# Optimization experiments

Measured on AMD Instinct MI355X. Metric: run time of the kernel, lower is better.

Reference implementation:

```python
import jax, jax.numpy as jnp
import numpy as np

# ---- static config (mirrors init_kwargs) ----
H, N, HKV = 32, 64, 8
HN = H * N            # model dim 2048
KV_DIM = HKV * N      # 512
B, T = 2, 1024
EPS = 1e-6
ROPE_THETA = 1.0e6
SPLITS_WAVGK = (96, 96, 64, 256, 64)   # xw, xa, xv, xg, xk lora ranks
SPLITS_RKV = (HN, KV_DIM, KV_DIM)


def rms_norm(x, w, eps=EPS):
    xf = x.astype(jnp.float32)
    var = jnp.mean(xf * xf, axis=-1, keepdims=True)
    return (w * (xf * jax.lax.rsqrt(var + eps))).astype(x.dtype)


def rotate_half(x):
    x1, x2 = jnp.split(x, 2, axis=-1)
    return jnp.concatenate((-x2, x1), axis=-1)


def apply_rope(q, k, cos, sin):
    # q:[B,T,H,N], k:[B,T,HKV,N], cos/sin:[B,T,N] -> unsqueeze head dim (unsqueeze_dim=2)
    cos = cos[:, :, None, :]
    sin = sin[:, :, None, :]
    return q * cos + rotate_half(q) * sin, k * cos + rotate_half(k) * sin


def rwkv7_recurrence(r, gk, k, v, a, b, S0):
    # fused_recurrent_rwkv7 (head_first=False). All inputs [B,T,H,N] fp32, S0 [B,H,N_key,N_val].
    # S_t = diag(exp(gk_t)) S_{t-1} + b_t (a_t^T S_{t-1}) + k_t v_t^T ;  o_t = r_t^T S_t
    def step(S, inp):
        r_t, w_t, k_t, v_t, a_t, b_t = inp
        sa = jnp.einsum('bhk,bhkv->bhv', a_t, S)
        S = (jnp.exp(w_t)[..., None] * S
             + k_t[..., None] * v_t[..., None, :]
             + b_t[..., None] * sa[..., None, :])
        o = jnp.einsum('bhk,bhkv->bhv', r_t, S)
        return S, o
    xs = tuple(jnp.swapaxes(t, 0, 1) for t in (r, gk, k, v, a, b))  # [T,B,H,N]
    S, o = jax.lax.scan(step, S0, xs)
    return jnp.swapaxes(o, 0, 1), S


def setup_inputs() -> dict:
    key = jax.random.key(0)
    ks = jax.random.split(key, 24)
    f32 = jnp.float32
    rn = lambda k, shape, s=1.0: jax.random.normal(k, shape, dtype=f32) * s

    x_in = rn(ks[0], (B, T, HN))
    v_first = rn(ks[1], (B, T, HKV, N))
    k_first = rn(ks[2], (B, T, HKV, N))
    state = jnp.zeros((B, H, N, N), f32)

    # real rope cache (faithful to get_batch_rope_cache output) at positions 0..T-1
    inv_freq = 1.0 / (ROPE_THETA ** (np.arange(0, N, 2, dtype=np.float32) / N))
    freqs = np.outer(np.arange(T, dtype=np.float32), inv_freq)  # [T, N/2]
    emb = np.concatenate([freqs, freqs], axis=-1)               # [T, N]
    calc_cos = jnp.broadcast_to(jnp.asarray(np.cos(emb), dtype=np.float32), (B, T, N))
    calc_sin = jnp.broadcast_to(jnp.asarray(np.sin(emb), dtype=np.float32), (B, T, N))

    wavgk1 = rn(ks[3], (HN, sum(SPLITS_WAVGK)), 0.02)
    w0 = rn(ks[4], (HN,), 0.5)
    w2 = rn(ks[5], (SPLITS_WAVGK[0], HN), 0.02)
    a0 = rn(ks[6], (HN,), 0.1)
    a2 = rn(ks[7], (SPLITS_WAVGK[1], HN), 0.02)
    v0 = rn(ks[8], (KV_DIM,), 0.1)
    v2 = rn(ks[9], (SPLITS_WAVGK[2], KV_DIM), 0.02)
    g2 = rn(ks[10], (SPLITS_WAVGK[3], HN), 0.02)
    k0 = rn(ks[11], (KV_DIM,), 0.1)
    k2 = rn(ks[12], (SPLITS_WAVGK[4], KV_DIM), 0.02)
    r_k = rn(ks[13], (H, N), 0.1)
    RKV = rn(ks[14], (HN, HN + 2 * KV_DIM), 0.02)   # fpx weight, dequantized form
    O = rn(ks[15], (HN, HN), 0.02)
    R_bias = rn(ks[16], (HN,), 0.02)
    K_bias = rn(ks[17], (KV_DIM,), 0.02)
    V_bias = rn(ks[18], (KV_DIM,), 0.02)
    ln_r = jnp.ones((N,), f32)
    ln_k = jnp.ones((N,), f32)
    ln1 = jnp.ones((HN,), f32)
    ln2 = jnp.ones((HN,), f32)

    return dict(x_in=x_in, v_first=v_first, k_first=k_first, state=state,
                calc_cos=calc_cos, calc_sin=calc_sin, wavgk1=wavgk1,
                w0=w0, w2=w2, a0=a0, a2=a2, v0=v0, v2=v2, g2=g2, k0=k0, k2=k2,
                r_k=r_k, RKV=RKV, O=O, R_bias=R_bias, K_bias=K_bias, V_bias=V_bias,
                ln_r=ln_r, ln_k=ln_k, ln1=ln1, ln2=ln2)


def reference(x_in, v_first, k_first, state, calc_cos, calc_sin, wavgk1,
              w0, w2, a0, a2, v0, v2, g2, k0, k2, r_k, RKV, O,
              R_bias, K_bias, V_bias, ln_r, ln_k, ln1, ln2):
    Bx, Tx, C = x_in.shape
    kv_repeat = HN // KV_DIM  # GQA repeat factor (4)

    x = rms_norm(x_in, ln1)
    xw, xa, xv, xg, xk = jnp.split(x @ wavgk1, np.cumsum(SPLITS_WAVGK)[:-1].tolist(), axis=-1)

    rkv = x @ RKV  # fpx_matmul -> dense matmul on dequantized weight
    r, k, v = jnp.split(rkv, np.cumsum(SPLITS_RKV)[:-1].tolist(), axis=-1)
    r = (r + R_bias).reshape(Bx, Tx, H, N)
    k = (k + K_bias).reshape(Bx, Tx, HKV, N)
    v = (v + V_bias).reshape(Bx, Tx, HKV, N)

    r = rms_norm(r, ln_r)
    k = rms_norm(k, ln_k)
    r, k = apply_rope(r, k, calc_cos, calc_sin)

    # layer_id = 1 (> 0): mix with first-layer value/key
    v = v + (v_first - v) * jax.nn.sigmoid(xv @ v2 + v0).reshape(Bx, Tx, HKV, N)
    k = k + (k_first - k) * jax.nn.sigmoid(xk @ k2 + k0).reshape(Bx, Tx, HKV, N)

    # repeat_kv: [B,T,HKV,N] -> [B,T,H,N] -> [B,T,HN]
    k = jnp.repeat(k, kv_repeat, axis=2).reshape(Bx, Tx, HN)
    v = jnp.repeat(v, kv_repeat, axis=2).reshape(Bx, Tx, HN)

    a = jax.nn.sigmoid(xa @ a2 + a0)  # in-context learning rate gate [B,T,HN]
    k4 = k.reshape(Bx, Tx, H, N)
    kk = (k4 / jnp.maximum(jnp.linalg.norm(k4, axis=-1, keepdims=True), 1e-12)).reshape(Bx, Tx, HN)

    w_log = -jax.nn.softplus(-(jnp.tanh(xw) @ w2 + w0)) - 0.5  # log-decay, <= -0.5
    k = k * (1.0 - w_log + a)
    aa = -kk
    bb = kk * a
    gk = -jnp.exp(w_log.astype(jnp.float32))  # passed to fused_recurrent_rwkv7 as log decay

    shp = (Bx, Tx, H, N)
    o, state_out = rwkv7_recurrence(
        r.reshape(shp).astype(jnp.float32), gk.reshape(shp),
        k.reshape(shp).astype(jnp.float32), v.reshape(shp).astype(jnp.float32),
        aa.reshape(shp).astype(jnp.float32), bb.reshape(shp).astype(jnp.float32),
        state.astype(jnp.float32))

    xx = o.reshape(Bx, Tx, HN) * (float(N) ** -0.5)
    bonus = ((r * k.reshape(shp) * r_k).sum(axis=-1, keepdims=True) * v.reshape(shp)).reshape(Bx, Tx, HN)
    xx = xx.astype(x_in.dtype) + bonus

    out = (xx * (jax.nn.sigmoid(xg) @ g2)) @ O  # fpx output projection
    x_new = x_in + out
    return rms_norm(x_new, ln2)
```

## Files before the change

kernel.cpp:

```cpp
#include <hip/hip_runtime.h>

typedef unsigned short u16;
typedef unsigned int u32;

using f32x4 = __attribute__((ext_vector_type(4))) float;
using bf16x8 = __attribute__((ext_vector_type(8))) __bf16;

#define HN 2048
#define KVD 512
#define TOKENS 2048
#define N1 3712
#define K2W 576
#define N2 7168

#define OFF_Y1   0ull
#define OFF_OO   0ull
#define OFF_XG   16777216ull
#define OFF_Y2   30408704ull
#define OFF_OUTR 30408704ull
#define OFF_BT1  89128960ull
#define OFF_XB   104333312ull
#define OFF_W2T  89128960ull
#define OFF_X2   97386496ull
#define OFF_OT   89128960ull
#define OFF_RR   112721920ull
#define OFF_DEC  129499136ull
#define OFF_KR   146276352ull
#define OFF_VV   163053568ull
#define OFF_AA   179830784ull
#define OFF_BB   196608000ull
#define OFF_PAB  213385216ull
#define OFF_PKR  230162432ull
#define WS_NEED  246939648ull

__device__ __forceinline__ u16 f2bf(float f) {
    u32 u = __float_as_uint(f);
    u32 r = u + 0x7fffu + ((u >> 16) & 1u);
    return (u16)(r >> 16);
}
__device__ __forceinline__ float sigm(float x) { return 1.f / (1.f + expf(-x)); }
__device__ __forceinline__ float wsum(float v) {
#pragma unroll
    for (int m = 32; m > 0; m >>= 1) v += __shfl_xor(v, m, 64);
    return v;
}
__device__ __forceinline__ float rowsum16(float v) {
    float t;
    t = __uint_as_float(__builtin_amdgcn_update_dpp(0, __float_as_uint(v), 0x121, 0xf, 0xf, true));
    v += t;
    t = __uint_as_float(__builtin_amdgcn_update_dpp(0, __float_as_uint(v), 0x122, 0xf, 0xf, true));
    v += t;
    t = __uint_as_float(__builtin_amdgcn_update_dpp(0, __float_as_uint(v), 0x124, 0xf, 0xf, true));
    v += t;
    t = __uint_as_float(__builtin_amdgcn_update_dpp(0, __float_as_uint(v), 0x128, 0xf, 0xf, true));
    v += t;
    return v;
}

typedef __attribute__((address_space(1))) const void glob_t;
typedef __attribute__((address_space(3))) void lds_t;
__device__ __forceinline__ void gload_lds16(const void* g, void* l) {
    __builtin_amdgcn_global_load_lds((glob_t*)g, (lds_t*)l, 16, 0, 0);
}

template<int OFF>
__device__ __forceinline__ float4 ds_read128(u32 a) {
    float4 r;
    asm volatile("ds_read_b128 %0, %1 offset:%2" : "=v"(r) : "v"(a), "i"(OFF));
    return r;
}
template<int OFF>
__device__ __forceinline__ uint4 ds_read128u(u32 a) {
    uint4 r;
    asm volatile("ds_read_b128 %0, %1 offset:%2" : "=v"(r) : "v"(a), "i"(OFF));
    return r;
}
template<int OFF>
__device__ __forceinline__ float ds_read32(u32 a) {
    float r;
    asm volatile("ds_read_b32 %0, %1 offset:%2" : "=v"(r) : "v"(a), "i"(OFF));
    return r;
}

__global__ __launch_bounds__(256) void k_prep_bt1(const float* __restrict__ wavgk1,
                                                  const float* __restrict__ RKV,
                                                  u16* __restrict__ BT1) {
    __shared__ float tile[64][65];
    const int bn = blockIdx.x >> 5;
    const int bk = blockIdx.x & 31;
    const int n0 = bn << 6, k0 = bk << 6;
    const int c = threadIdx.x & 63, q = threadIdx.x >> 6;
#pragma unroll
    for (int i = 0; i < 16; ++i) {
        const int r = (q << 4) + i;
        float v = 0.f;
        if (bn < 9)       v = wavgk1[(size_t)(k0 + r) * 576 + n0 + c];
        else if (bn < 57) v = RKV[(size_t)(k0 + r) * 3072 + (n0 + c - 576)];
        tile[r][c] = v;
    }
    __syncthreads();
#pragma unroll
    for (int i = 0; i < 16; ++i) {
        const int rw = (q << 4) + i;
        BT1[(size_t)(n0 + rw) * 2048 + k0 + c] = f2bf(tile[c][rw]);
    }
}

__global__ __launch_bounds__(256) void k_prep_w2t(const float* __restrict__ w2, const float* __restrict__ a2,
                                                  const float* __restrict__ g2, const float* __restrict__ v2,
                                                  const float* __restrict__ k2, u16* __restrict__ W2T) {
    __shared__ float tile[64][65];
    const int bx = blockIdx.x;
    const int bn = bx / 9, bc = bx - bn * 9;
    const int n0 = bn << 6, c0 = bc << 6;
    const int cc = threadIdx.x & 63, q = threadIdx.x >> 6;
#pragma unroll
    for (int i = 0; i < 16; ++i) {
        const int r = (q << 4) + i;
        const int c = c0 + r;
        const int n = n0 + cc;
        float v = 0.f;
        if (n0 < 2048)      { if (c < 96)              v = w2[(size_t)c * 2048 + n]; }
        else if (n0 < 4096) { if (c >= 96 && c < 192)  v = a2[(size_t)(c - 96) * 2048 + (n - 2048)]; }
        else if (n0 < 6144) { if (c >= 192 && c < 448) v = g2[(size_t)(c - 192) * 2048 + (n - 4096)]; }
        else if (n0 < 6656) { if (c >= 448 && c < 512) v = v2[(size_t)(c - 448) * 512 + (n - 6144)]; }
        else                { if (c >= 512)            v = k2[(size_t)(c - 512) * 512 + (n - 6656)]; }
        tile[r][cc] = v;
    }
    __syncthreads();
#pragma unroll
    for (int i = 0; i < 16; ++i) {
        const int rw = (q << 4) + i;
        W2T[(size_t)(n0 + rw) * 576 + c0 + cc] = f2bf(tile[cc][rw]);
    }
}

__global__ __launch_bounds__(256) void k_prep_ot(const float* __restrict__ O, u16* __restrict__ OT) {
    __shared__ float tile[64][65];
    const int bn = blockIdx.x >> 5, bk = blockIdx.x & 31;
    const int n0 = bn << 6, k0 = bk << 6;
    const int c = threadIdx.x & 63, q = threadIdx.x >> 6;
#pragma unroll
    for (int i = 0; i < 16; ++i) {
        const int r = (q << 4) + i;
        tile[r][c] = O[(size_t)(k0 + r) * 2048 + n0 + c];
    }
    __syncthreads();
#pragma unroll
    for (int i = 0; i < 16; ++i) {
        const int rw = (q << 4) + i;
        OT[(size_t)(n0 + rw) * 2048 + k0 + c] = f2bf(tile[c][rw]);
    }
}

__global__ __launch_bounds__(256) void k_rms1(const float* __restrict__ X,
                                              const float* __restrict__ ln1,
                                              u16* __restrict__ XB) {
    const int t = blockIdx.x, tid = threadIdx.x;
    const float* row = X + ((size_t)t << 11);
    float4 v0 = *(const float4*)(row + tid * 8);
    float4 v1 = *(const float4*)(row + tid * 8 + 4);
    float ss = v0.x*v0.x + v0.y*v0.y + v0.z*v0.z + v0.w*v0.w
             + v1.x*v1.x + v1.y*v1.y + v1.z*v1.z + v1.w*v1.w;
    ss = wsum(ss);
    __shared__ float red[4];
    if ((tid & 63) == 0) red[tid >> 6] = ss;
    __syncthreads();
    float scale = rsqrtf((red[0] + red[1] + red[2] + red[3]) * (1.f / 2048.f) + 1e-6f);
    float4 w0_ = *(const float4*)(ln1 + tid * 8);
    float4 w1_ = *(const float4*)(ln1 + tid * 8 + 4);
    u16* o = XB + ((size_t)t << 11) + tid * 8;
    o[0] = f2bf(v0.x * scale * w0_.x); o[1] = f2bf(v0.y * scale * w0_.y);
    o[2] = f2bf(v0.z * scale * w0_.z); o[3] = f2bf(v0.w * scale * w0_.w);
    o[4] = f2bf(v1.x * scale * w1_.x); o[5] = f2bf(v1.y * scale * w1_.y);
    o[6] = f2bf(v1.z * scale * w1_.z); o[7] = f2bf(v1.w * scale * w1_.w);
}

__global__ __launch_bounds__(256) void k_gemm(const u16* __restrict__ A,
                                              const u16* __restrict__ Bt,
                                              float* __restrict__ C,
                                              int M, int N, int K) {
    __shared__ __align__(16) u16 tA[4096];
    __shared__ __align__(16) u16 tB[4096];
    const int tid = threadIdx.x;
    const int w = tid >> 6, l = tid & 63;
    const int bm = blockIdx.x << 7, bn = blockIdx.y << 7;
    const int wm = (w >> 1) << 6, wn = (w & 1) << 6;
    const int lrow = l >> 2;
    const int lk = (((l & 3) ^ ((l >> 3) & 3)) << 3);
    f32x4 acc[4][4] = {};
    const size_t rA0 = (size_t)(bm + (w << 4) + lrow) * K;
    const size_t rA1 = (size_t)(bm + ((w + 4) << 4) + lrow) * K;
    const size_t rB0 = (size_t)(bn + (w << 4) + lrow) * K;
    const size_t rB1 = (size_t)(bn + ((w + 4) << 4) + lrow) * K;
    const int frow = l & 15;
    const int koff = (((l >> 4) ^ ((l >> 1) & 3)) << 3);
    for (int kt = 0; kt < K; kt += 32) {
        gload_lds16(A + rA0 + kt + lk, &tA[w << 9]);
        gload_lds16(A + rA1 + kt + lk, &tA[2048 + (w << 9)]);
        gload_lds16(Bt + rB0 + kt + lk, &tB[w << 9]);
        gload_lds16(Bt + rB1 + kt + lk, &tB[2048 + (w << 9)]);
        __syncthreads();
        bf16x8 av[4], bv[4];
#pragma unroll
        for (int i = 0; i < 4; ++i) {
            av[i] = *(const bf16x8*)&tA[((wm + (i << 4) + frow) << 5) + koff];
            bv[i] = *(const bf16x8*)&tB[((wn + (i << 4) + frow) << 5) + koff];
        }
#pragma unroll
        for (int i = 0; i < 4; ++i)
#pragma unroll
            for (int j = 0; j < 4; ++j)
                acc[i][j] = __builtin_amdgcn_mfma_f32_16x16x32_bf16(av[i], bv[j], acc[i][j], 0, 0, 0);
        __syncthreads();
    }
    const int crow = bm + wm + ((l >> 4) << 2);
    const int ccol = bn + wn + (l & 15);
#pragma unroll
    for (int i = 0; i < 4; ++i)
#pragma unroll
        for (int j = 0; j < 4; ++j)
#pragma unroll
            for (int jj = 0; jj < 4; ++jj)
                C[(size_t)(crow + (i << 4) + jj) * N + ccol + (j << 4)] = acc[i][j][jj];
}

__global__ __launch_bounds__(256) void k_gemm2(const u16* __restrict__ A,
                                               const u16* __restrict__ Bt,
                                               float* __restrict__ C) {
    __shared__ __align__(16) u16 tA[4096];
    __shared__ __align__(16) u16 tB[4096];
    const int tid = threadIdx.x;
    const int w = tid >> 6, l = tid & 63;
    const int by = blockIdx.y;
    int c0, K;
    if (by < 16)      { c0 = 0;   K = 96; }
    else if (by < 32) { c0 = 96;  K = 96; }
    else if (by < 48) { c0 = 192; K = 256; }
    else if (by < 52) { c0 = 448; K = 64; }
    else              { c0 = 512; K = 64; }
    const int n0 = by << 7;
    const int bm = blockIdx.x << 7;
    const int wm = (w >> 1) << 6, wn = (w & 1) << 6;
    const int lrow = l >> 2;
    const int lk = (((l & 3) ^ ((l >> 3) & 3)) << 3);
    f32x4 acc[4][4] = {};
    const size_t rA0 = (size_t)(bm + (w << 4) + lrow) * 576 + c0;
    const size_t rA1 = (size_t)(bm + ((w + 4) << 4) + lrow) * 576 + c0;
    const size_t rB0 = (size_t)(n0 + (w << 4) + lrow) * 576 + c0;
    const size_t rB1 = (size_t)(n0 + ((w + 4) << 4) + lrow) * 576 + c0;
    const int frow = l & 15;
    const int koff = (((l >> 4) ^ ((l >> 1) & 3)) << 3);
    for (int kt = 0; kt < K; kt += 32) {
        gload_lds16(A + rA0 + kt + lk, &tA[w << 9]);
        gload_lds16(A + rA1 + kt + lk, &tA[2048 + (w << 9)]);
        gload_lds16(Bt + rB0 + kt + lk, &tB[w << 9]);
        gload_lds16(Bt + rB1 + kt + lk, &tB[2048 + (w << 9)]);
        __syncthreads();
        bf16x8 av[4], bv[4];
#pragma unroll
        for (int i = 0; i < 4; ++i) {
            av[i] = *(const bf16x8*)&tA[((wm + (i << 4) + frow) << 5) + koff];
            bv[i] = *(const bf16x8*)&tB[((wn + (i << 4) + frow) << 5) + koff];
        }
#pragma unroll
        for (int i = 0; i < 4; ++i)
#pragma unroll
            for (int j = 0; j < 4; ++j)
                acc[i][j] = __builtin_amdgcn_mfma_f32_16x16x32_bf16(av[i], bv[j], acc[i][j], 0, 0, 0);
        __syncthreads();
    }
    const int crow = bm + wm + ((l >> 4) << 2);
    const int ccol = n0 + wn + (l & 15);
#pragma unroll
    for (int i = 0; i < 4; ++i)
#pragma unroll
        for (int j = 0; j < 4; ++j)
#pragma unroll
            for (int jj = 0; jj < 4; ++jj)
                C[(size_t)(crow + (i << 4) + jj) * N2 + ccol + (j << 4)] = acc[i][j][jj];
}

__global__ __launch_bounds__(256) void k_prep_x2(const float* __restrict__ Y1, u16* __restrict__ X2) {
    int idx = blockIdx.x * 256 + threadIdx.x;
    int t = idx / 576, c = idx - t * 576;
    const float* y1 = Y1 + (size_t)t * N1;
    float v;
    if (c < 96)       v = tanhf(y1[c]);
    else if (c < 192) v = y1[c];
    else if (c < 448) v = sigm(y1[c + 64]);
    else if (c < 512) v = y1[c - 256];
    else              v = y1[c];
    X2[idx] = f2bf(v);
}

__global__ __launch_bounds__(256) void k_prep_rec(
    const float* __restrict__ Y1, const float* __restrict__ Y2,
    const float* __restrict__ v_first, const float* __restrict__ k_first,
    const float* __restrict__ cosb, const float* __restrict__ sinb,
    const float* __restrict__ w0, const float* __restrict__ a0,
    const float* __restrict__ v0b, const float* __restrict__ k0b,
    const float* __restrict__ R_bias, const float* __restrict__ K_bias,
    const float* __restrict__ V_bias, const float* __restrict__ ln_r,
    const float* __restrict__ ln_k,
    float* __restrict__ RR, float* __restrict__ DEC, float* __restrict__ KR,
    float* __restrict__ VV, u32* __restrict__ PAB, u32* __restrict__ PKR) {
    const int t = blockIdx.x, tid = threadIdx.x;
    const int ww = tid >> 6, lane = tid & 63;
    const float* y1 = Y1 + (size_t)t * N1;
    const float* y2 = Y2 + (size_t)t * N2;
    const float cs = cosb[t * 64 + lane];
    const float sn = sinb[t * 64 + lane];
    const float sign = lane < 32 ? -1.f : 1.f;
    const size_t tb = (size_t)t << 11;
    __shared__ float kkv[512], vkv[512];
    float rsave[8];
#pragma unroll
    for (int i = 0; i < 8; ++i) {
        int h = ww * 8 + i, c = h * 64 + lane;
        float rr = y1[576 + c] + R_bias[c];
        float ssq = wsum(rr * rr);
        float rn = ln_r[lane] * rr * rsqrtf(ssq * (1.f / 64.f) + 1e-6f);
        float rot = sign * __shfl(rn, lane ^ 32, 64);
        rsave[i] = rn * cs + rot * sn;
        RR[tb + c] = rsave[i];
    }
#pragma unroll
    for (int i = 0; i < 2; ++i) {
        int j = ww * 2 + i, c = j * 64 + lane;
        float kr = y1[2624 + c] + K_bias[c];
        float ssq = wsum(kr * kr);
        float kn = ln_k[lane] * kr * rsqrtf(ssq * (1.f / 64.f) + 1e-6f);
        float rot = sign * __shfl(kn, lane ^ 32, 64);
        float krope = kn * cs + rot * sn;
        float ksig = sigm(y2[6656 + c] + k0b[c]);
        kkv[c] = krope + (k_first[(size_t)t * 512 + c] - krope) * ksig;
        float vr = y1[3136 + c] + V_bias[c];
        float vsig = sigm(y2[6144 + c] + v0b[c]);
        vkv[c] = vr + (v_first[(size_t)t * 512 + c] - vr) * vsig;
    }
    __syncthreads();
#pragma unroll
    for (int i = 0; i < 8; ++i) {
        int h = ww * 8 + i, c = h * 64 + lane;
        int ckv = (h >> 2) * 64 + lane;
        float kb = kkv[ckv], vb = vkv[ckv];
        float a_ = sigm(y2[2048 + c] + a0[c]);
        float wr = y2[c] + w0[c];
        float z = -wr;
        float sp = fmaxf(z, 0.f) + log1pf(expf(-fabsf(z)));
        float w_log = -sp - 0.5f;
        float ssq = wsum(kb * kb);
        float kk = kb / fmaxf(sqrtf(ssq), 1e-12f);
        const float kr2 = kb * (1.f - w_log + a_);
        DEC[tb + c] = expf(-expf(w_log));
        KR[tb + c] = kr2;
        VV[tb + c] = vb;
        PAB[tb + c] = (u32)f2bf(-kk) | ((u32)f2bf(kk * a_) << 16);
        PKR[tb + c] = (u32)f2bf(kr2) | ((u32)f2bf(rsave[i]) << 16);
    }
}

__global__ __launch_bounds__(256, 1) void k_recv16(
    const float* __restrict__ DECp, const u32* __restrict__ PABp,
    const u32* __restrict__ PKRp, const float* __restrict__ VVp,
    const float* __restrict__ S0, float* __restrict__ OO) {
    __shared__ __align__(16) float cbuf[2][4][32][64];
    const int tid = threadIdx.x;
    const int wl = tid >> 6;
    const int lane = tid & 63;
    const int vl = lane >> 4;
    const int kq = lane & 15;
    const int quarter = blockIdx.x & 3;
    const int ch = blockIdx.x >> 2;
    const int vcol = (quarter << 4) + (wl << 2) + vl;
    const size_t cb = ((size_t)(ch >> 5) * 1024 * 2048) + ((size_t)(ch & 31) << 6);

    const float* s0 = S0 + ((size_t)ch << 12);
    float L0 = s0[((kq << 2) + 0) * 64 + vcol];
    float L1 = s0[((kq << 2) + 1) * 64 + vcol];
    float L2 = s0[((kq << 2) + 2) * 64 + vcol];
    float L3 = s0[((kq << 2) + 3) * 64 + vcol];

    const int trow = (wl << 2) + vl;

#define STG(B, T0)                                                             \
    {                                                                          \
        const size_t g0 = cb + (size_t)((T0) + trow) * 2048 + (kq << 2);       \
        const size_t g1 = cb + (size_t)((T0) + 16 + trow) * 2048 + (kq << 2);  \
        float* lb = &cbuf[B][0][0][0] + (wl << 8);                             \
        gload_lds16(DECp + g0, lb);                                            \
        gload_lds16(DECp + g1, lb + 1024);                                     \
        gload_lds16(PABp + g0, lb + 2048);                                     \
        gload_lds16(PABp + g1, lb + 3072);                                     \
        gload_lds16(PKRp + g0, lb + 4096);                                     \
        gload_lds16(PKRp + g1, lb + 5120);                                     \
        gload_lds16(VVp + g0, lb + 6144);                                      \
        gload_lds16(VVp + g1, lb + 7168);                                      \
    }

    const u32 base0 = (u32)(size_t)(void*)&cbuf[0][0][0][0];
    const u32 aA0 = base0 + (kq << 4);
    const u32 aV0 = base0 + 24576 + (vcol << 2);

    float4 cDa0, cDa1, cDb0, cDb1;
    uint4 cPAa0, cPAa1, cPAb0, cPAb1, cPKa0, cPKa1, cPKb0, cPKb1;
    float cV[32];

#define LD2(S_, G)                                                             \
    cD##S_##0 = ds_read128<(G) * 512>(aAb);                                    \
    cD##S_##1 = ds_read128<(G) * 512 + 256>(aAb);                              \
    cPA##S_##0 = ds_read128u<8192 + (G) * 512>(aAb);                           \
    cPA##S_##1 = ds_read128u<8192 + (G) * 512 + 256>(aAb);                     \
    cPK##S_##0 = ds_read128u<16384 + (G) * 512>(aAb);                          \
    cPK##S_##1 = ds_read128u<16384 + (G) * 512 + 256>(aAb);

#define VRD(J) cV[J] = ds_read32<(J) * 256>(aVb);
#define VRD8(J) VRD(J) VRD((J)+1) VRD((J)+2) VRD((J)+3) VRD((J)+4) VRD((J)+5) VRD((J)+6) VRD((J)+7)

#define WAIT6 asm volatile("s_waitcnt lgkmcnt(6)" ::: "memory");               \
    __builtin_amdgcn_sched_barrier(0);
#define WAIT0 asm volatile("s_waitcnt lgkmcnt(0)" ::: "memory");               \
    __builtin_amdgcn_sched_barrier(0);

#define UNP_LO(u) __uint_as_float((u) << 16)
#define UNP_HI(u) __uint_as_float((u) & 0xffff0000u)

#define STEP1(D4, pa, pk, Vsj, T)                                              \
    {                                                                          \
        const float Ax = UNP_LO(pa.x), Ay = UNP_LO(pa.y),                      \
                    Az = UNP_LO(pa.z), Aw = UNP_LO(pa.w);                      \
        const float Bx = UNP_HI(pa.x), By = UNP_HI(pa.y),                      \
                    Bz = UNP_HI(pa.z), Bw = UNP_HI(pa.w);                      \
        const float Kx = UNP_LO(pk.x), Ky = UNP_LO(pk.y),                      \
                    Kz = UNP_LO(pk.z), Kw = UNP_LO(pk.w);                      \
        const float Rx = UNP_HI(pk.x), Ry = UNP_HI(pk.y),                      \
                    Rz = UNP_HI(pk.z), Rw = UNP_HI(pk.w);                      \
        float sp = fmaf(L1, Ay, L0 * Ax) + fmaf(L3, Aw, L2 * Az);              \
        const float sa = rowsum16(sp);                                         \
        L0 = fmaf(Bx, sa, fmaf(Kx, Vsj, L0 * D4.x));                           \
        L1 = fmaf(By, sa, fmaf(Ky, Vsj, L1 * D4.y));                           \
        L2 = fmaf(Bz, sa, fmaf(Kz, Vsj, L2 * D4.z));                           \
        L3 = fmaf(Bw, sa, fmaf(Kw, Vsj, L3 * D4.w));                           \
        float op = fmaf(L1, Ry, L0 * Rx) + fmaf(L3, Rw, L2 * Rz);              \
        const float o = rowsum16(op);                                          \
        if (kq == 0) OO[cb + ((size_t)(T) << 11) + vcol] = o;                  \
    }

#define STEP2(S_, G)                                                           \
    STEP1(cD##S_##0, cPA##S_##0, cPK##S_##0, cV[2 * (G)], tbase + 2 * (G));    \
    STEP1(cD##S_##1, cPA##S_##1, cPK##S_##1, cV[2 * (G) + 1], tbase + 2 * (G) + 1);

#define PAIR(G)                                                                \
    LD2(b, (G) + 1) WAIT6 STEP2(a, G) LD2(a, (G) + 2) WAIT6 STEP2(b, (G) + 1)

    STG(0, 0);
    __syncthreads();

    for (int c = 0; c < 32; ++c) {
        const int b = c & 1;
        if (c < 31) STG(b ^ 1, (c + 1) << 5);
        const u32 aAb = aA0 + b * 32768;
        const u32 aVb = aV0 + b * 32768;
        const int tbase = c << 5;
        VRD8(0) VRD8(8) VRD8(16) VRD8(24)
        WAIT0
        LD2(a, 0)
        PAIR(0) PAIR(2) PAIR(4) PAIR(6) PAIR(8) PAIR(10) PAIR(12)
        LD2(b, 15) WAIT6 STEP2(a, 14) WAIT0 STEP2(b, 15)
        __syncthreads();
    }
#undef PAIR
#undef STEP2
#undef STEP1
#undef UNP_LO
#undef UNP_HI
#undef WAIT0
#undef WAIT6
#undef VRD8
#undef VRD
#undef LD2
#undef STG
}

__global__ __launch_bounds__(256) void k_gate(
    const float* __restrict__ OOp, const float* __restrict__ RRp,
    const float* __restrict__ KRp, const float* __restrict__ VVp,
    const float* __restrict__ Y2, const float* __restrict__ r_k,
    u16* __restrict__ XG) {
    const int t = blockIdx.x, tid = threadIdx.x;
    const int ww = tid >> 6, lane = tid & 63;
    const size_t tb = (size_t)t << 11;
#pragma unroll
    for (int i = 0; i < 8; ++i) {
        int c = (ww * 8 + i) * 64 + lane;
        float pr = RRp[tb + c] * KRp[tb + c] * r_k[c];
        float dot = wsum(pr);
        float xx = OOp[tb + c] * 0.125f + dot * VVp[tb + c];
        float g = Y2[(size_t)t * N2 + 4096 + c];
        XG[tb + c] = f2bf(xx * g);
    }
}

__global__ __launch_bounds__(256) void k_final(const float* __restrict__ x_in,
                                               const float* __restrict__ OUTR,
                                               const float* __restrict__ ln2,
                                               float* __restrict__ out) {
    const int t = blockIdx.x, tid = threadIdx.x;
    const float* xr = x_in + ((size_t)t << 11);
    const float* orow = OUTR + ((size_t)t << 11);
    float4 a0 = *(const float4*)(xr + tid * 8);
    float4 a1 = *(const float4*)(xr + tid * 8 + 4);
    float4 b0 = *(const float4*)(orow + tid * 8);
    float4 b1 = *(const float4*)(orow + tid * 8 + 4);
    float v[8] = {a0.x + b0.x, a0.y + b0.y, a0.z + b0.z, a0.w + b0.w,
                  a1.x + b1.x, a1.y + b1.y, a1.z + b1.z, a1.w + b1.w};
    float ss = 0.f;
#pragma unroll
    for (int i = 0; i < 8; ++i) ss = fmaf(v[i], v[i], ss);
    ss = wsum(ss);
    __shared__ float red[4];
    if ((tid & 63) == 0) red[tid >> 6] = ss;
    __syncthreads();
    float scale = rsqrtf((red[0] + red[1] + red[2] + red[3]) * (1.f / 2048.f) + 1e-6f);
    float* o = out + ((size_t)t << 11) + tid * 8;
#pragma unroll
    for (int i = 0; i < 8; ++i) o[i] = ln2[tid * 8 + i] * v[i] * scale;
}

extern "C" void kernel_launch(void* const* d_in, const int* in_sizes, int n_in,
                              void* d_out, int out_size, void* d_ws, size_t ws_size,
                              hipStream_t stream) {
    const float* x_in    = (const float*)d_in[0];
    const float* v_first = (const float*)d_in[1];
    const float* k_first = (const float*)d_in[2];
    const float* state   = (const float*)d_in[3];
    const float* cosb    = (const float*)d_in[4];
    const float* sinb    = (const float*)d_in[5];
    const float* wavgk1  = (const float*)d_in[6];
    const float* w0      = (const float*)d_in[7];
    const float* w2      = (const float*)d_in[8];
    const float* a0      = (const float*)d_in[9];
    const float* a2      = (const float*)d_in[10];
    const float* v0      = (const float*)d_in[11];
    const float* v2      = (const float*)d_in[12];
    const float* g2      = (const float*)d_in[13];
    const float* k0      = (const float*)d_in[14];
    const float* k2      = (const float*)d_in[15];
    const float* r_k     = (const float*)d_in[16];
    const float* RKV     = (const float*)d_in[17];
    const float* O       = (const float*)d_in[18];
    const float* R_bias  = (const float*)d_in[19];
    const float* K_bias  = (const float*)d_in[20];
    const float* V_bias  = (const float*)d_in[21];
    const float* ln_r    = (const float*)d_in[22];
    const float* ln_k    = (const float*)d_in[23];
    const float* ln1     = (const float*)d_in[24];
    const float* ln2     = (const float*)d_in[25];

    if (ws_size < WS_NEED) return;

    char* ws = (char*)d_ws;
    u16*   BT1  = (u16*)(ws + OFF_BT1);
    u16*   W2T  = (u16*)(ws + OFF_W2T);
    u16*   OT   = (u16*)(ws + OFF_OT);
    u16*   XB   = (u16*)(ws + OFF_XB);
    float* Y1   = (float*)(ws + OFF_Y1);
    u16*   X2   = (u16*)(ws + OFF_X2);
    float* Y2   = (float*)(ws + OFF_Y2);
    float* RR   = (float*)(ws + OFF_RR);
    float* DEC  = (float*)(ws + OFF_DEC);
    float* KR   = (float*)(ws + OFF_KR);
    float* VV   = (float*)(ws + OFF_VV);
    u32*   PAB  = (u32*)(ws + OFF_PAB);
    u32*   PKR  = (u32*)(ws + OFF_PKR);
    float* OO   = (float*)(ws + OFF_OO);
    u16*   XG   = (u16*)(ws + OFF_XG);
    float* OUTR = (float*)(ws + OFF_OUTR);

    k_prep_bt1<<<1856, 256, 0, stream>>>(wavgk1, RKV, BT1);
    k_rms1<<<2048, 256, 0, stream>>>(x_in, ln1, XB);
    k_gemm<<<dim3(16, 29), 256, 0, stream>>>(XB, BT1, Y1, 2048, N1, 2048);
    k_prep_w2t<<<1008, 256, 0, stream>>>(w2, a2, g2, v2, k2, W2T);
    k_prep_x2<<<4608, 256, 0, stream>>>(Y1, X2);
    k_gemm2<<<dim3(16, 56), 256, 0, stream>>>(X2, W2T, Y2);
    k_prep_rec<<<2048, 256, 0, stream>>>(Y1, Y2, v_first, k_first, cosb, sinb,
                                         w0, a0, v0, k0, R_bias, K_bias, V_bias,
                                         ln_r, ln_k, RR, DEC, KR, VV, PAB, PKR);
    k_prep_ot<<<1024, 256, 0, stream>>>(O, OT);
    k_recv16<<<256, 256, 0, stream>>>(DEC, PAB, PKR, VV, state, OO);
    k_gate<<<2048, 256, 0, stream>>>(OO, RR, KR, VV, Y2, r_k, XG);
    k_gemm<<<dim3(16, 16), 256, 0, stream>>>(XG, OT, OUTR, 2048, 2048, 2048);
    k_final<<<2048, 256, 0, stream>>>(x_in, OUTR, ln2, (float*)d_out);
}
```

Before: 376.9 us.

## Store first GEMM output in bf16 and precompute bonus dot products in prep

The first projection GEMM now writes its output as bf16 instead of fp32, halving the Y1 write and the later reads by the prep kernels. The per-head r·k·r_k bonus dot product is computed once in k_prep_rec and stored as a small per-token, per-head array, so the RR and KR fp32 buffers are no longer written or read. The gate kernel becomes a vectorized elementwise pass that loads the precomputed dot. This trades some precision, since Y1 is rounded to bf16 before the norms, sigmoid and tanh, for less memory traffic.

```diff
diff --git a/kernel.cpp b/kernel.cpp
--- a/kernel.cpp
+++ b/kernel.cpp
@@ -31,12 +31,16 @@
 #define OFF_BB   196608000ull
 #define OFF_PAB  213385216ull
 #define OFF_PKR  230162432ull
-#define WS_NEED  246939648ull
+#define OFF_DOT  246939648ull
+#define WS_NEED  247201792ull
 
 __device__ __forceinline__ u16 f2bf(float f) {
     u32 u = __float_as_uint(f);
     u32 r = u + 0x7fffu + ((u >> 16) & 1u);
     return (u16)(r >> 16);
+}
+__device__ __forceinline__ float bf2f(u16 b) {
+    return __uint_as_float(((u32)b) << 16);
 }
 __device__ __forceinline__ float sigm(float x) { return 1.f / (1.f + expf(-x)); }
 __device__ __forceinline__ float wsum(float v) {
@@ -223,6 +227,55 @@
 #pragma unroll
             for (int jj = 0; jj < 4; ++jj)
                 C[(size_t)(crow + (i << 4) + jj) * N + ccol + (j << 4)] = acc[i][j][jj];
+}
+
+__global__ __launch_bounds__(256) void k_gemmb(const u16* __restrict__ A,
+                                               const u16* __restrict__ Bt,
+                                               u16* __restrict__ C,
+                                               int M, int N, int K) {
+    __shared__ __align__(16) u16 tA[4096];
+    __shared__ __align__(16) u16 tB[4096];
+    const int tid = threadIdx.x;
+    const int w = tid >> 6, l = tid & 63;
+    const int bm = blockIdx.x << 7, bn = blockIdx.y << 7;
+    const int wm = (w >> 1) << 6, wn = (w & 1) << 6;
+    const int lrow = l >> 2;
+    const int lk = (((l & 3) ^ ((l >> 3) & 3)) << 3);
+    f32x4 acc[4][4] = {};
+    const size_t rA0 = (size_t)(bm + (w << 4) + lrow) * K;
+    const size_t rA1 = (size_t)(bm + ((w + 4) << 4) + lrow) * K;
+    const size_t rB0 = (size_t)(bn + (w << 4) + lrow) * K;
+    const size_t rB1 = (size_t)(bn + ((w + 4) << 4) + lrow) * K;
+    const int frow = l & 15;
+    const int koff = (((l >> 4) ^ ((l >> 1) & 3)) << 3);
+    for (int kt = 0; kt < K; kt += 32) {
+        gload_lds16(A + rA0 + kt + lk, &tA[w << 9]);
+        gload_lds16(A + rA1 + kt + lk, &tA[2048 + (w << 9)]);
+        gload_lds16(Bt + rB0 + kt + lk, &tB[w << 9]);
+        gload_lds16(Bt + rB1 + kt + lk, &tB[2048 + (w << 9)]);
+        __syncthreads();
+        bf16x8 av[4], bv[4];
+#pragma unroll
+        for (int i = 0; i < 4; ++i) {
+            av[i] = *(const bf16x8*)&tA[((wm + (i << 4) + frow) << 5) + koff];
+            bv[i] = *(const bf16x8*)&tB[((wn + (i << 4) + frow) << 5) + koff];
+        }
+#pragma unroll
+        for (int i = 0; i < 4; ++i)
+#pragma unroll
+            for (int j = 0; j < 4; ++j)
+                acc[i][j] = __builtin_amdgcn_mfma_f32_16x16x32_bf16(av[i], bv[j], acc[i][j], 0, 0, 0);
+        __syncthreads();
+    }
+    const int crow = bm + wm + ((l >> 4) << 2);
+    const int ccol = bn + wn + (l & 15);
+#pragma unroll
+    for (int i = 0; i < 4; ++i)
+#pragma unroll
+        for (int j = 0; j < 4; ++j)
+#pragma unroll
+            for (int jj = 0; jj < 4; ++jj)
+                C[(size_t)(crow + (i << 4) + jj) * N + ccol + (j << 4)] = f2bf(acc[i][j][jj]);
 }
 
 __global__ __launch_bounds__(256) void k_gemm2(const u16* __restrict__ A,
@@ -281,33 +334,33 @@
                 C[(size_t)(crow + (i << 4) + jj) * N2 + ccol + (j << 4)] = acc[i][j][jj];
 }
 
-__global__ __launch_bounds__(256) void k_prep_x2(const float* __restrict__ Y1, u16* __restrict__ X2) {
+__global__ __launch_bounds__(256) void k_prep_x2(const u16* __restrict__ Y1, u16* __restrict__ X2) {
     int idx = blockIdx.x * 256 + threadIdx.x;
     int t = idx / 576, c = idx - t * 576;
-    const float* y1 = Y1 + (size_t)t * N1;
+    const u16* y1 = Y1 + (size_t)t * N1;
     float v;
-    if (c < 96)       v = tanhf(y1[c]);
-    else if (c < 192) v = y1[c];
-    else if (c < 448) v = sigm(y1[c + 64]);
-    else if (c < 512) v = y1[c - 256];
-    else              v = y1[c];
+    if (c < 96)       v = tanhf(bf2f(y1[c]));
+    else if (c < 192) v = bf2f(y1[c]);
+    else if (c < 448) v = sigm(bf2f(y1[c + 64]));
+    else if (c < 512) v = bf2f(y1[c - 256]);
+    else              v = bf2f(y1[c]);
     X2[idx] = f2bf(v);
 }
 
 __global__ __launch_bounds__(256) void k_prep_rec(
-    const float* __restrict__ Y1, const float* __restrict__ Y2,
+    const u16* __restrict__ Y1, const float* __restrict__ Y2,
     const float* __restrict__ v_first, const float* __restrict__ k_first,
     const float* __restrict__ cosb, const float* __restrict__ sinb,
     const float* __restrict__ w0, const float* __restrict__ a0,
     const float* __restrict__ v0b, const float* __restrict__ k0b,
     const float* __restrict__ R_bias, const float* __restrict__ K_bias,
     const float* __restrict__ V_bias, const float* __restrict__ ln_r,
-    const float* __restrict__ ln_k,
-    float* __restrict__ RR, float* __restrict__ DEC, float* __restrict__ KR,
-    float* __restrict__ VV, u32* __restrict__ PAB, u32* __restrict__ PKR) {
+    const float* __restrict__ ln_k, const float* __restrict__ r_k,
+    float* __restrict__ DEC, float* __restrict__ VV,
+    u32* __restrict__ PAB, u32* __restrict__ PKR, float* __restrict__ DOT) {
     const int t = blockIdx.x, tid = threadIdx.x;
     const int ww = tid >> 6, lane = tid & 63;
-    const float* y1 = Y1 + (size_t)t * N1;
+    const u16* y1 = Y1 + (size_t)t * N1;
     const float* y2 = Y2 + (size_t)t * N2;
     const float cs = cosb[t * 64 + lane];
     const float sn = sinb[t * 64 + lane];
@@ -318,24 +371,23 @@
 #pragma unroll
     for (int i = 0; i < 8; ++i) {
         int h = ww * 8 + i, c = h * 64 + lane;
-        float rr = y1[576 + c] + R_bias[c];
+        float rr = bf2f(y1[576 + c]) + R_bias[c];
         float ssq = wsum(rr * rr);
         float rn = ln_r[lane] * rr * rsqrtf(ssq * (1.f / 64.f) + 1e-6f);
         float rot = sign * __shfl(rn, lane ^ 32, 64);
         rsave[i] = rn * cs + rot * sn;
-        RR[tb + c] = rsave[i];
     }
 #pragma unroll
     for (int i = 0; i < 2; ++i) {
         int j = ww * 2 + i, c = j * 64 + lane;
-        float kr = y1[2624 + c] + K_bias[c];
+        float kr = bf2f(y1[2624 + c]) + K_bias[c];
         float ssq = wsum(kr * kr);
         float kn = ln_k[lane] * kr * rsqrtf(ssq * (1.f / 64.f) + 1e-6f);
         float rot = sign * __shfl(kn, lane ^ 32, 64);
         float krope = kn * cs + rot * sn;
         float ksig = sigm(y2[6656 + c] + k0b[c]);
         kkv[c] = krope + (k_first[(size_t)t * 512 + c] - krope) * ksig;
-        float vr = y1[3136 + c] + V_bias[c];
+        float vr = bf2f(y1[3136 + c]) + V_bias[c];
         float vsig = sigm(y2[6144 + c] + v0b[c]);
         vkv[c] = vr + (v_first[(size_t)t * 512 + c] - vr) * vsig;
     }
@@ -353,15 +405,17 @@
         float ssq = wsum(kb * kb);
         float kk = kb / fmaxf(sqrtf(ssq), 1e-12f);
         const float kr2 = kb * (1.f - w_log + a_);
+        const float rrv = rsave[i];
         DEC[tb + c] = expf(-expf(w_log));
-        KR[tb + c] = kr2;
         VV[tb + c] = vb;
         PAB[tb + c] = (u32)f2bf(-kk) | ((u32)f2bf(kk * a_) << 16);
-        PKR[tb + c] = (u32)f2bf(kr2) | ((u32)f2bf(rsave[i]) << 16);
-    }
-}
-
-__global__ __launch_bounds__(256, 1) void k_recv16(
+        PKR[tb + c] = (u32)f2bf(kr2) | ((u32)f2bf(rrv) << 16);
+        const float dsum = wsum(rrv * kr2 * r_k[c]);
+        if (lane == 0) DOT[((size_t)t << 5) + h] = dsum;
+    }
+}
+
+__global__ __launch_bounds__(256, 1) void k_recv17(
     const float* __restrict__ DECp, const u32* __restrict__ PABp,
     const u32* __restrict__ PKRp, const float* __restrict__ VVp,
     const float* __restrict__ S0, float* __restrict__ OO) {
@@ -484,22 +538,34 @@
 }
 
 __global__ __launch_bounds__(256) void k_gate(
-    const float* __restrict__ OOp, const float* __restrict__ RRp,
-    const float* __restrict__ KRp, const float* __restrict__ VVp,
-    const float* __restrict__ Y2, const float* __restrict__ r_k,
+    const float* __restrict__ OOp, const float* __restrict__ VVp,
+    const float* __restrict__ DOT, const float* __restrict__ Y2,
     u16* __restrict__ XG) {
     const int t = blockIdx.x, tid = threadIdx.x;
-    const int ww = tid >> 6, lane = tid & 63;
     const size_t tb = (size_t)t << 11;
-#pragma unroll
-    for (int i = 0; i < 8; ++i) {
-        int c = (ww * 8 + i) * 64 + lane;
-        float pr = RRp[tb + c] * KRp[tb + c] * r_k[c];
-        float dot = wsum(pr);
-        float xx = OOp[tb + c] * 0.125f + dot * VVp[tb + c];
-        float g = Y2[(size_t)t * N2 + 4096 + c];
-        XG[tb + c] = f2bf(xx * g);
-    }
+    const int c0 = tid << 3;
+    const float dot = DOT[((size_t)t << 5) + (tid >> 3)];
+    float4 o0 = *(const float4*)(OOp + tb + c0);
+    float4 o1 = *(const float4*)(OOp + tb + c0 + 4);
+    float4 v0 = *(const float4*)(VVp + tb + c0);
+    float4 v1 = *(const float4*)(VVp + tb + c0 + 4);
+    const float* g = Y2 + (size_t)t * N2 + 4096 + c0;
+    float4 g0 = *(const float4*)(g);
+    float4 g1 = *(const float4*)(g + 4);
+    const float x0 = fmaf(o0.x, 0.125f, dot * v0.x) * g0.x;
+    const float x1 = fmaf(o0.y, 0.125f, dot * v0.y) * g0.y;
+    const float x2 = fmaf(o0.z, 0.125f, dot * v0.z) * g0.z;
+    const float x3 = fmaf(o0.w, 0.125f, dot * v0.w) * g0.w;
+    const float x4 = fmaf(o1.x, 0.125f, dot * v1.x) * g1.x;
+    const float x5 = fmaf(o1.y, 0.125f, dot * v1.y) * g1.y;
+    const float x6 = fmaf(o1.z, 0.125f, dot * v1.z) * g1.z;
+    const float x7 = fmaf(o1.w, 0.125f, dot * v1.w) * g1.w;
+    uint4 pk;
+    pk.x = (u32)f2bf(x0) | ((u32)f2bf(x1) << 16);
+    pk.y = (u32)f2bf(x2) | ((u32)f2bf(x3) << 16);
+    pk.z = (u32)f2bf(x4) | ((u32)f2bf(x5) << 16);
+    pk.w = (u32)f2bf(x6) | ((u32)f2bf(x7) << 16);
+    *(uint4*)(XG + tb + c0) = pk;
 }
 
 __global__ __launch_bounds__(256) void k_final(const float* __restrict__ x_in,
@@ -565,31 +631,30 @@
     u16*   W2T  = (u16*)(ws + OFF_W2T);
     u16*   OT   = (u16*)(ws + OFF_OT);
     u16*   XB   = (u16*)(ws + OFF_XB);
-    float* Y1   = (float*)(ws + OFF_Y1);
+    u16*   Y1   = (u16*)(ws + OFF_Y1);
     u16*   X2   = (u16*)(ws + OFF_X2);
     float* Y2   = (float*)(ws + OFF_Y2);
-    float* RR   = (float*)(ws + OFF_RR);
     float* DEC  = (float*)(ws + OFF_DEC);
-    float* KR   = (float*)(ws + OFF_KR);
     float* VV   = (float*)(ws + OFF_VV);
     u32*   PAB  = (u32*)(ws + OFF_PAB);
     u32*   PKR  = (u32*)(ws + OFF_PKR);
+    float* DOT  = (float*)(ws + OFF_DOT);
     float* OO   = (float*)(ws + OFF_OO);
     u16*   XG   = (u16*)(ws + OFF_XG);
     float* OUTR = (float*)(ws + OFF_OUTR);
 
     k_prep_bt1<<<1856, 256, 0, stream>>>(wavgk1, RKV, BT1);
     k_rms1<<<2048, 256, 0, stream>>>(x_in, ln1, XB);
-    k_gemm<<<dim3(16, 29), 256, 0, stream>>>(XB, BT1, Y1, 2048, N1, 2048);
+    k_gemmb<<<dim3(16, 29), 256, 0, stream>>>(XB, BT1, Y1, 2048, N1, 2048);
     k_prep_w2t<<<1008, 256, 0, stream>>>(w2, a2, g2, v2, k2, W2T);
     k_prep_x2<<<4608, 256, 0, stream>>>(Y1, X2);
     k_gemm2<<<dim3(16, 56), 256, 0, stream>>>(X2, W2T, Y2);
     k_prep_rec<<<2048, 256, 0, stream>>>(Y1, Y2, v_first, k_first, cosb, sinb,
                                          w0, a0, v0, k0, R_bias, K_bias, V_bias,
-                                         ln_r, ln_k, RR, DEC, KR, VV, PAB, PKR);
+                                         ln_r, ln_k, r_k, DEC, VV, PAB, PKR, DOT);
     k_prep_ot<<<1024, 256, 0, stream>>>(O, OT);
-    k_recv16<<<256, 256, 0, stream>>>(DEC, PAB, PKR, VV, state, OO);
-    k_gate<<<2048, 256, 0, stream>>>(OO, RR, KR, VV, Y2, r_k, XG);
+    k_recv17<<<256, 256, 0, stream>>>(DEC, PAB, PKR, VV, state, OO);
+    k_gate<<<2048, 256, 0, stream>>>(OO, VV, DOT, Y2, XG);
     k_gemm<<<dim3(16, 16), 256, 0, stream>>>(XG, OT, OUTR, 2048, 2048, 2048);
     k_final<<<2048, 256, 0, stream>>>(x_in, OUTR, ln2, (float*)d_out);
 }
```

Measured after the change: 361.1 us. 4.2% less time.
